# Kernel tuning notes

Hardware: AMD Instinct MI355X
Metric: run time of the kernel (lower is better)

The kernel has to match this reference:

```python
import jax, jax.numpy as jnp
import numpy as np

B, T, S, A = 8, 256, 16, 1
H, NH, L, NI, TIME, TMAX = 1024, 16, 6, 4096, 8, 512
NEG = -10000.0


def _ln(x, g, b, eps=1e-5):
    m = jnp.mean(x, -1, keepdims=True)
    v = jnp.mean((x - m) ** 2, -1, keepdims=True)
    return (x - m) * jax.lax.rsqrt(v + eps) * g + b


def setup_inputs() -> dict:
    key = jax.random.key(0)
    ks = iter(jax.random.split(key, 64))
    w = lambda *s: 0.02 * jax.random.normal(next(ks), s, jnp.float32)
    inp = {
        'states': jax.random.normal(next(ks), (B, T, S), jnp.float32),
        'actions': jax.random.normal(next(ks), (B, T, A), jnp.float32),
        'rtgs': jax.random.normal(next(ks), (B, T, 1), jnp.float32),
        'attention_mask': jnp.ones((B, T, 1), jnp.float32),
        'state_mean': jnp.zeros((S,), jnp.float32),
        'state_std': jnp.ones((S,), jnp.float32),
        'W_es': w(S, H), 'b_es': jnp.zeros((H,)),
        'W_ea': w(A, H), 'b_ea': jnp.zeros((H,)),
        'W_er': w(1, H), 'b_er': jnp.zeros((H,)),
        'E_t': w(TMAX, TIME),
        'W_ts': w(H + TIME, H), 'b_ts': jnp.zeros((H,)),
        'W_ta': w(H + TIME, H), 'b_ta': jnp.zeros((H,)),
        'W_tr': w(H + TIME, H), 'b_tr': jnp.zeros((H,)),
        'eln_g': jnp.ones((H,)), 'eln_b': jnp.zeros((H,)),
        'ln1_g': jnp.ones((L, H)), 'ln1_b': jnp.zeros((L, H)),
        'ln2_g': jnp.ones((L, H)), 'ln2_b': jnp.zeros((L, H)),
        'Wq': w(L, H, H), 'bq': jnp.zeros((L, H)),
        'Wk': w(L, H, H), 'bk': jnp.zeros((L, H)),
        'Wv': w(L, H, H), 'bv': jnp.zeros((L, H)),
        'Wo': w(L, H, H), 'bo': jnp.zeros((L, H)),
        'W1': w(L, H, NI), 'b1': jnp.zeros((L, NI)),
        'W2': w(L, NI, H), 'b2': jnp.zeros((L, H)),
        'W_pa': w(H, A), 'b_pa': jnp.zeros((A,)),
        'timesteps': jax.random.randint(next(ks), (B, T), 0, TMAX),
    }
    return inp


def _forward(states, actions, rtgs, attention_mask, state_mean, state_std,
             W_es, b_es, W_ea, b_ea, W_er, b_er, E_t,
             W_ts, b_ts, W_ta, b_ta, W_tr, b_tr, eln_g, eln_b,
             ln1_g, ln1_b, ln2_g, ln2_b, Wq, bq, Wk, bk, Wv, bv, Wo, bo,
             W1, b1, W2, b2, W_pa, b_pa, timesteps):
    T3 = 3 * T
    dh = H // NH
    s = (states - state_mean) / (state_std + 1e-9)
    te = E_t[timesteps]                                   # [B,T,8]
    se = jnp.concatenate([s @ W_es + b_es, te], -1) @ W_ts + b_ts
    ae = jnp.concatenate([actions @ W_ea + b_ea, te], -1) @ W_ta + b_ta
    re = jnp.concatenate([rtgs @ W_er + b_er, te], -1) @ W_tr + b_tr
    # interleave (rtg, state, action) per timestep -> [B, 3T, H]
    x = jnp.stack([re, se, ae], axis=2).reshape(B, T3, H)
    x = _ln(x, eln_g, eln_b)

    timestep_mask = jnp.max(attention_mask, axis=-1)      # [B,T]
    pad = (1.0 - jnp.repeat(timestep_mask, 3, axis=1)) * NEG  # [B,3T]
    pad = pad[:, None, None, :]
    causal = jnp.tril(jnp.ones((T3, T3), bool))

    def block(x, p):
        (l1g, l1b, wq, bqv, wk, bkv, wv, bvv, wo, bov,
         l2g, l2b, w1, b1v, w2, b2v) = p
        h = _ln(x, l1g, l1b)
        def heads(w, b):
            return (h @ w + b).reshape(B, T3, NH, dh).transpose(0, 2, 1, 3)
        q, k, v = heads(wq, bqv), heads(wk, bkv), heads(wv, bvv)
        att = jnp.einsum('bhqd,bhkd->bhqk', q, k) / jnp.sqrt(jnp.float32(dh))
        att = jnp.where(causal, att, jnp.asarray(NEG, att.dtype)) + pad
        att = jax.nn.softmax(att, axis=-1)
        y = jnp.einsum('bhqk,bhkd->bhqd', att, v)
        y = y.transpose(0, 2, 1, 3).reshape(B, T3, H) @ wo + bov
        x = x + y
        m = _ln(x, l2g, l2b)
        x = x + jax.nn.gelu(m @ w1 + b1v, approximate=False) @ w2 + b2v
        return x, None

    stacked = (ln1_g, ln1_b, Wq, bq, Wk, bk, Wv, bv, Wo, bo,
               ln2_g, ln2_b, W1, b1, W2, b2)
    x, _ = jax.lax.scan(block, x, stacked)

    x = x.reshape(B, T, 3, H)
    action_preds = x[:, :, 1] @ W_pa + b_pa               # state-token positions
    return action_preds


def reference(states, actions, rtgs, attention_mask, state_mean, state_std,
              W_es, b_es, W_ea, b_ea, W_er, b_er, E_t,
              W_ts, b_ts, W_ta, b_ta, W_tr, b_tr, eln_g, eln_b,
              ln1_g, ln1_b, ln2_g, ln2_b, Wq, bq, Wk, bk, Wv, bv, Wo, bo,
              W1, b1, W2, b2, W_pa, b_pa, timesteps):
    return _forward(states, actions, rtgs, attention_mask, state_mean, state_std,
                    W_es, b_es, W_ea, b_ea, W_er, b_er, E_t,
                    W_ts, b_ts, W_ta, b_ta, W_tr, b_tr, eln_g, eln_b,
                    ln1_g, ln1_b, ln2_g, ln2_b, Wq, bq, Wk, bk, Wv, bv, Wo, bo,
                    W1, b1, W2, b2, W_pa, b_pa, timesteps)
```

## Files before the change

### kernel.cpp

```cpp
#include <hip/hip_runtime.h>
#include <math.h>

#define B_    8
#define T_    256
#define S_    16
#define H_    1024
#define NH_   16
#define L_    6
#define NI_   4096
#define TIME_ 8
#define T3_   768
#define DH_   64
#define BT_   2048
#define ROWS_ 6144
#define KE_   1032
#define KEP_  1056
#define NEGV  (-10000.0f)

typedef unsigned short u16;
typedef short bf16x8 __attribute__((ext_vector_type(8)));
typedef float f32x4 __attribute__((ext_vector_type(4)));

__device__ __forceinline__ float bf2f(u16 u) {
    union { unsigned int i; float f; } x; x.i = ((unsigned int)u) << 16; return x.f;
}
__device__ __forceinline__ u16 f2bf(float f) {
    union { float f; unsigned int i; } x; x.f = f;
    unsigned int r = x.i + 0x7FFFu + ((x.i >> 16) & 1u);
    return (u16)(r >> 16);
}
__device__ __forceinline__ float gelu_fast(float x) {
    float y = 0.7978845608028654f * (x + 0.044715f * x * x * x);
    float e = __expf(2.0f * y);
    float t = 1.0f - 2.0f / (e + 1.0f);
    return 0.5f * x * (1.0f + t);
}

__device__ __forceinline__ void gll16(const u16* g, u16* l) {
    __builtin_amdgcn_global_load_lds(
        (const __attribute__((address_space(1))) unsigned int*)g,
        (__attribute__((address_space(3))) unsigned int*)l,
        16, 0, 0);
}

template <int EPI, int BM>
__device__ __forceinline__ void mgemm_core(
    const u16* __restrict__ A, const u16* __restrict__ Bt,
    const float* __restrict__ bias, float* __restrict__ outf,
    u16* __restrict__ outb, const float* __restrict__ res,
    int N, int K, int koff, int klen, bool addb)
{
    constexpr int MT = (BM == 128) ? 4 : 2;
    __shared__ u16 Als[2][BM * 32];
    __shared__ u16 Bls[2][128 * 32];
    const int tid = threadIdx.x;

    const int nbx = N >> 7;
    const int bid = blockIdx.x;
    const int G = nbx << 3;
    const int grp = bid / G;
    const int g = bid - grp * G;
    const int bm = (grp * 8 + (g & 7)) * BM;
    const int bn = (g >> 3) * 128;

    const int lane = tid & 63;
    const int w = tid >> 6;
    const int wr = (BM == 128) ? (w >> 1) : (w & 1);
    const int wc = (BM == 128) ? (w & 1) : (w >> 1);
    const int lrow = lane & 15;
    const int lk = lane >> 4;

    f32x4 acc[MT][4] = {};

    auto stage = [&](int buf, int kk) {
        if (BM == 128) {
            #pragma unroll
            for (int s = 0; s < 2; ++s) {
                const int gb = w * 64 + s * 256;
                const int j = gb >> 7, m0 = gb & 127;
                gll16(A + (size_t)(bm + m0 + lane) * K + kk + j * 8, Als[buf] + gb * 8);
            }
        } else {
            gll16(A + (size_t)(bm + lane) * K + kk + w * 8, Als[buf] + w * 64 * 8);
        }
        #pragma unroll
        for (int s = 0; s < 2; ++s) {
            const int gb = w * 64 + s * 256;
            const int j = gb >> 7, m0 = gb & 127;
            gll16(Bt + (size_t)(bn + m0 + lane) * K + kk + j * 8, Bls[buf] + gb * 8);
        }
    };

    const int niter = klen >> 5;
    stage(0, koff);
    for (int i = 0; i < niter; ++i) {
        __syncthreads();
        if (i + 1 < niter) stage((i + 1) & 1, koff + (i + 1) * 32);
        const bf16x8* Af = (const bf16x8*)Als[i & 1];
        const bf16x8* Bf = (const bf16x8*)Bls[i & 1];
        bf16x8 af[MT], bfr[4];
        #pragma unroll
        for (int tm = 0; tm < MT; ++tm)
            af[tm] = Af[lk * BM + wr * (MT * 16) + tm * 16 + lrow];
        #pragma unroll
        for (int tn = 0; tn < 4; ++tn)
            bfr[tn] = Bf[lk * 128 + wc * 64 + tn * 16 + lrow];
        #pragma unroll
        for (int tm = 0; tm < MT; ++tm)
            #pragma unroll
            for (int tn = 0; tn < 4; ++tn)
                acc[tm][tn] = __builtin_amdgcn_mfma_f32_16x16x32_bf16(
                    af[tm], bfr[tn], acc[tm][tn], 0, 0, 0);
    }

    int cg[4]; float bv[4];
    #pragma unroll
    for (int tn = 0; tn < 4; ++tn) {
        cg[tn] = bn + wc * 64 + tn * 16 + lrow;
        bv[tn] = addb ? bias[cg[tn]] : 0.0f;
    }
    #pragma unroll
    for (int tm = 0; tm < MT; ++tm) {
        const int rbase = bm + wr * (MT * 16) + tm * 16 + lk * 4;
        #pragma unroll
        for (int r = 0; r < 4; ++r) {
            const size_t rowoff = (size_t)(rbase + r) * N;
            #pragma unroll
            for (int tn = 0; tn < 4; ++tn) {
                float v = acc[tm][tn][r] + bv[tn];
                const size_t idx = rowoff + cg[tn];
                if (EPI == 0) outf[idx] = v;
                else if (EPI == 1) outf[idx] = v + res[idx];
                else if (EPI == 2) outb[idx] = f2bf(v);
                else if (EPI == 3) { outb[idx] = f2bf(gelu_fast(v)); }
                else { unsafeAtomicAdd(outf + idx, v); }
            }
        }
    }
}

template <int EPI, int BM>
__global__ __launch_bounds__(256) void mgemm(
    const u16* __restrict__ A, const u16* __restrict__ Bt,
    const float* __restrict__ bias, float* __restrict__ outf,
    u16* __restrict__ outb, const float* __restrict__ res,
    int N, int K)
{
    mgemm_core<EPI, BM>(A, Bt, bias, outf, outb, res, N, K, 0, K, true);
}

template <int EPI, int BM>
__global__ __launch_bounds__(256) void mgemm_sk(
    const u16* __restrict__ A, const u16* __restrict__ Bt,
    const float* __restrict__ bias, float* __restrict__ outf,
    u16* __restrict__ outb, const float* __restrict__ res,
    int N, int K, int nsplit)
{
    const int split = blockIdx.y;
    const int klen = K / nsplit;
    mgemm_core<EPI, BM>(A, Bt, bias, outf, outb, res, N, K,
                        split * klen, klen, split == 0);
}

__global__ __launch_bounds__(256) void mgemm_embed(
    const u16* __restrict__ U, const u16* __restrict__ Wt,
    const float* __restrict__ b0, const float* __restrict__ b1,
    const float* __restrict__ b2, float* __restrict__ out)
{
    const int z = blockIdx.z;
    const float* bias = (z == 0) ? b0 : (z == 1) ? b1 : b2;
    mgemm_core<0, 64>(U + (size_t)z * BT_ * KEP_, Wt + (size_t)z * H_ * KEP_,
                      bias, out + (size_t)z * BT_ * H_, nullptr, nullptr,
                      H_, KEP_, 0, KEP_, true);
}

__device__ __forceinline__ void convT_core(
    const float* __restrict__ W, u16* __restrict__ Wt, int K, int N, int Kpad)
{
    __shared__ float tile[32][65];
    const int k0 = blockIdx.y * 32, n0 = blockIdx.x * 64;
    const int tid = threadIdx.x;
    #pragma unroll
    for (int p = 0; p < 2; ++p) {
        const int kr = (tid >> 4) + p * 16;
        const int nc = (tid & 15) * 4;
        const int k = k0 + kr;
        float4 v = make_float4(0.f, 0.f, 0.f, 0.f);
        if (k < K) v = *(const float4*)(W + (size_t)k * N + n0 + nc);
        tile[kr][nc + 0] = v.x; tile[kr][nc + 1] = v.y;
        tile[kr][nc + 2] = v.z; tile[kr][nc + 3] = v.w;
    }
    __syncthreads();
    #pragma unroll
    for (int p = 0; p < 2; ++p) {
        const int idx = tid + p * 256;
        const int n = idx >> 3, kq = (idx & 7) * 4;
        ushort4 o;
        o.x = f2bf(tile[kq + 0][n]); o.y = f2bf(tile[kq + 1][n]);
        o.z = f2bf(tile[kq + 2][n]); o.w = f2bf(tile[kq + 3][n]);
        *(ushort4*)(Wt + (size_t)(n0 + n) * Kpad + k0 + kq) = o;
    }
}

__global__ __launch_bounds__(256) void convTv(
    const float* __restrict__ W, u16* __restrict__ Wt, int K, int N, int Kpad)
{
    convT_core(W, Wt, K, N, Kpad);
}

__global__ __launch_bounds__(256) void convT_embed(
    const float* __restrict__ W0, const float* __restrict__ W1,
    const float* __restrict__ W2, u16* __restrict__ Wt)
{
    const int z = blockIdx.z;
    const float* W = (z == 0) ? W0 : (z == 1) ? W1 : W2;
    convT_core(W, Wt + (size_t)z * H_ * KEP_, KE_, H_, KEP_);
}

__global__ __launch_bounds__(256) void convT4v(
    const float* __restrict__ Wq, const float* __restrict__ Wk,
    const float* __restrict__ Wv, const float* __restrict__ Wo,
    const float* __restrict__ bq, const float* __restrict__ bk,
    const float* __restrict__ bv,
    u16* __restrict__ WQKVt, u16* __restrict__ Wot, float* __restrict__ bqkv)
{
    const int z = blockIdx.z;
    const float* W = (z == 0) ? Wq : (z == 1) ? Wk : (z == 2) ? Wv : Wo;
    u16* Wt = (z == 3) ? Wot : WQKVt + (size_t)z * H_ * H_;
    convT_core(W, Wt, H_, H_, H_);
    if (blockIdx.x == 0 && blockIdx.y == 0 && z < 3) {
        const float* bsrc = (z == 0) ? bq : (z == 1) ? bk : bv;
        #pragma unroll
        for (int u = 0; u < 4; ++u) {
            int i = threadIdx.x + u * 256;
            bqkv[z * H_ + i] = bsrc[i];
        }
    }
}

__global__ __launch_bounds__(256) void embed_pre_kernel(
    const float* __restrict__ states, const float* __restrict__ actions,
    const float* __restrict__ rtgs, const float* __restrict__ mean,
    const float* __restrict__ stdv, const float* __restrict__ W_es,
    const float* __restrict__ b_es, const float* __restrict__ W_ea,
    const float* __restrict__ b_ea, const float* __restrict__ W_er,
    const float* __restrict__ b_er, const float* __restrict__ E_t,
    const int* __restrict__ timesteps,
    u16* __restrict__ Us, u16* __restrict__ Ua, u16* __restrict__ Ur)
{
    const int bt  = blockIdx.x;
    const int tid = threadIdx.x;
    __shared__ float sn[S_];
    __shared__ float tev[TIME_];
    if (tid < S_) sn[tid] = (states[bt * S_ + tid] - mean[tid]) / (stdv[tid] + 1e-9f);
    if (tid < TIME_) {
        int ts = timesteps[bt];
        tev[tid] = E_t[ts * TIME_ + tid];
    }
    __syncthreads();
    const float av = actions[bt];
    const float rv = rtgs[bt];
    const size_t rowo = (size_t)bt * KEP_;
    #pragma unroll
    for (int u = 0; u < 4; ++u) {
        int n = tid + u * 256;
        float accs = b_es[n];
        #pragma unroll
        for (int i = 0; i < S_; ++i) accs += sn[i] * W_es[i * H_ + n];
        Us[rowo + n] = f2bf(accs);
        Ua[rowo + n] = f2bf(av * W_ea[n] + b_ea[n]);
        Ur[rowo + n] = f2bf(rv * W_er[n] + b_er[n]);
    }
    if (tid < TIME_) {
        u16 tv = f2bf(tev[tid]);
        Us[rowo + H_ + tid] = tv;
        Ua[rowo + H_ + tid] = tv;
        Ur[rowo + H_ + tid] = tv;
    }
    if (tid < KEP_ - KE_) {
        Us[rowo + KE_ + tid] = 0;
        Ua[rowo + KE_ + tid] = 0;
        Ur[rowo + KE_ + tid] = 0;
    }
}

template <bool BF16OUT>
__device__ __forceinline__ void ln_body(const float* __restrict__ src,
                                        const float* __restrict__ g,
                                        const float* __restrict__ b,
                                        void* __restrict__ dst,
                                        float* red, int tid)
{
    float v[4];
    #pragma unroll
    for (int u = 0; u < 4; ++u) v[u] = src[tid + u * 256];
    float s = v[0] + v[1] + v[2] + v[3];
    red[tid] = s; __syncthreads();
    for (int off = 128; off > 0; off >>= 1) {
        if (tid < off) red[tid] += red[tid + off];
        __syncthreads();
    }
    const float mean = red[0] * (1.0f / H_);
    __syncthreads();
    float ss = 0.0f;
    #pragma unroll
    for (int u = 0; u < 4; ++u) { float d = v[u] - mean; ss += d * d; }
    red[tid] = ss; __syncthreads();
    for (int off = 128; off > 0; off >>= 1) {
        if (tid < off) red[tid] += red[tid + off];
        __syncthreads();
    }
    const float var = red[0] * (1.0f / H_);
    const float rs = rsqrtf(var + 1e-5f);
    #pragma unroll
    for (int u = 0; u < 4; ++u) {
        int col = tid + u * 256;
        float y = (v[u] - mean) * rs * g[col] + b[col];
        if (BF16OUT) ((u16*)dst)[col] = f2bf(y);
        else ((float*)dst)[col] = y;
    }
}

__global__ __launch_bounds__(256) void ln_bf16_kernel(
    const float* __restrict__ X, const float* __restrict__ g,
    const float* __restrict__ b, u16* __restrict__ Y)
{
    __shared__ float red[256];
    const size_t row = blockIdx.x;
    ln_body<true>(X + row * H_, g, b, Y + row * H_, red, threadIdx.x);
}

__global__ __launch_bounds__(256) void interleave_eln_kernel(
    const float* __restrict__ RE, const float* __restrict__ SE,
    const float* __restrict__ AE, const float* __restrict__ g,
    const float* __restrict__ b, float* __restrict__ X)
{
    __shared__ float red[256];
    const int row = blockIdx.x;
    const int bi = row / T3_;
    const int rem = row % T3_;
    const int t = rem / 3, slot = rem % 3;
    const float* src = (slot == 0 ? RE : (slot == 1 ? SE : AE)) + (size_t)(bi * T_ + t) * H_;
    ln_body<false>(src, g, b, X + (size_t)row * H_, red, threadIdx.x);
}

__global__ __launch_bounds__(256) void attn_kernel(
    const u16* __restrict__ QKV, const float* __restrict__ amask,
    u16* __restrict__ Y)
{
    const int qt = blockIdx.x;
    const int h  = blockIdx.y;
    const int b  = blockIdx.z;
    const int tid = threadIdx.x;
    const int lane = tid & 63, w = tid >> 6;
    const int l15 = lane & 15, quad = lane >> 4;

    __shared__ u16 Kls[64][72];
    __shared__ u16 Vt[64][72];
    __shared__ u16 Pls[4][16][72];
    __shared__ float padv[64];

    const u16* Qbase = QKV + (size_t)b * T3_ * 3072 + h * 64;
    const u16* Kbase = Qbase + 1024;
    const u16* Vbase = Qbase + 2048;

    bf16x8 qf[2];
    {
        const u16* qp = Qbase + (size_t)(qt * 64 + w * 16 + l15) * 3072 + quad * 8;
        qf[0] = *(const bf16x8*)qp;
        qf[1] = *(const bf16x8*)(qp + 32);
    }

    float m_i[4], l_i[4];
    f32x4 o[4] = {};
    #pragma unroll
    for (int r = 0; r < 4; ++r) { m_i[r] = -3.0e30f; l_i[r] = 0.0f; }

    const int qr0 = qt * 64 + w * 16 + quad * 4;

    for (int kt = 0; kt <= qt; ++kt) {
        #pragma unroll
        for (int s = 0; s < 2; ++s) {
            const int c = tid + s * 256;
            const int tok = c >> 3, cb = c & 7;
            const size_t go = (size_t)(kt * 64 + tok) * 3072 + cb * 8;
            *(uint4*)&Kls[tok][cb * 8] = *(const uint4*)(Kbase + go);
            uint4 vv = *(const uint4*)(Vbase + go);
            const u16* vs = (const u16*)&vv;
            #pragma unroll
            for (int j = 0; j < 8; ++j) Vt[cb * 8 + j][tok] = vs[j];
        }
        if (tid < 64)
            padv[tid] = (1.0f - amask[b * T_ + (kt * 64 + tid) / 3]) * NEGV;
        __syncthreads();

        f32x4 sacc[4];
        #pragma unroll
        for (int nt = 0; nt < 4; ++nt) {
            bf16x8 kf0 = *(const bf16x8*)&Kls[nt * 16 + l15][quad * 8];
            bf16x8 kf1 = *(const bf16x8*)&Kls[nt * 16 + l15][32 + quad * 8];
            f32x4 z = {};
            z = __builtin_amdgcn_mfma_f32_16x16x32_bf16(qf[0], kf0, z, 0, 0, 0);
            sacc[nt] = __builtin_amdgcn_mfma_f32_16x16x32_bf16(qf[1], kf1, z, 0, 0, 0);
        }

        float sv[4][4];
        float rmax[4] = {-3.0e30f, -3.0e30f, -3.0e30f, -3.0e30f};
        #pragma unroll
        for (int nt = 0; nt < 4; ++nt) {
            const int jc = kt * 64 + nt * 16 + l15;
            const float pv = padv[nt * 16 + l15];
            #pragma unroll
            for (int r = 0; r < 4; ++r) {
                float v = (jc <= qr0 + r) ? sacc[nt][r] * 0.125f : NEGV;
                v += pv;
                sv[nt][r] = v;
                rmax[r] = fmaxf(rmax[r], v);
            }
        }
        #pragma unroll
        for (int m = 1; m < 16; m <<= 1)
            #pragma unroll
            for (int r = 0; r < 4; ++r)
                rmax[r] = fmaxf(rmax[r], __shfl_xor(rmax[r], m, 64));
        float al[4], rsum[4];
        #pragma unroll
        for (int r = 0; r < 4; ++r) {
            const float mn = fmaxf(m_i[r], rmax[r]);
            al[r] = __expf(m_i[r] - mn);
            m_i[r] = mn;
            float sum = 0.0f;
            #pragma unroll
            for (int nt = 0; nt < 4; ++nt) {
                float p = __expf(sv[nt][r] - mn);
                sv[nt][r] = p; sum += p;
            }
            rsum[r] = sum;
        }
        #pragma unroll
        for (int m = 1; m < 16; m <<= 1)
            #pragma unroll
            for (int r = 0; r < 4; ++r)
                rsum[r] += __shfl_xor(rsum[r], m, 64);
        #pragma unroll
        for (int r = 0; r < 4; ++r)
            l_i[r] = l_i[r] * al[r] + rsum[r];

        #pragma unroll
        for (int nt = 0; nt < 4; ++nt)
            #pragma unroll
            for (int r = 0; r < 4; ++r)
                Pls[w][quad * 4 + r][nt * 16 + l15] = f2bf(sv[nt][r]);
        #pragma unroll
        for (int dt = 0; dt < 4; ++dt)
            #pragma unroll
            for (int r = 0; r < 4; ++r)
                o[dt][r] *= al[r];

        bf16x8 pf0 = *(const bf16x8*)&Pls[w][l15][quad * 8];
        bf16x8 pf1 = *(const bf16x8*)&Pls[w][l15][32 + quad * 8];
        #pragma unroll
        for (int dt = 0; dt < 4; ++dt) {
            bf16x8 vf0 = *(const bf16x8*)&Vt[dt * 16 + l15][quad * 8];
            bf16x8 vf1 = *(const bf16x8*)&Vt[dt * 16 + l15][32 + quad * 8];
            o[dt] = __builtin_amdgcn_mfma_f32_16x16x32_bf16(pf0, vf0, o[dt], 0, 0, 0);
            o[dt] = __builtin_amdgcn_mfma_f32_16x16x32_bf16(pf1, vf1, o[dt], 0, 0, 0);
        }
        __syncthreads();
    }

    #pragma unroll
    for (int r = 0; r < 4; ++r) {
        const float inv = 1.0f / l_i[r];
        const size_t row = (size_t)b * T3_ + qt * 64 + w * 16 + quad * 4 + r;
        #pragma unroll
        for (int dt = 0; dt < 4; ++dt)
            Y[row * H_ + h * 64 + dt * 16 + l15] = f2bf(o[dt][r] * inv);
    }
}

__global__ __launch_bounds__(256) void head_kernel(
    const float* __restrict__ X, const float* __restrict__ W_pa,
    const float* __restrict__ b_pa, float* __restrict__ out)
{
    __shared__ float red[256];
    const int row = blockIdx.x;
    const int b = row / T_, t = row % T_;
    const float* x = X + ((size_t)b * T3_ + 3 * t + 1) * H_;
    const int tid = threadIdx.x;
    float s = 0.0f;
    #pragma unroll
    for (int u = 0; u < 4; ++u) {
        int col = tid + u * 256;
        s += x[col] * W_pa[col];
    }
    red[tid] = s; __syncthreads();
    for (int off = 128; off > 0; off >>= 1) {
        if (tid < off) red[tid] += red[tid + off];
        __syncthreads();
    }
    if (tid == 0) out[row] = red[0] + b_pa[0];
}

extern "C" void kernel_launch(void* const* d_in, const int* in_sizes, int n_in,
                              void* d_out, int out_size, void* d_ws, size_t ws_size,
                              hipStream_t stream)
{
    const float* states  = (const float*)d_in[0];
    const float* actions = (const float*)d_in[1];
    const float* rtgs    = (const float*)d_in[2];
    const float* amask   = (const float*)d_in[3];
    const float* smean   = (const float*)d_in[4];
    const float* sstd    = (const float*)d_in[5];
    const float* W_es    = (const float*)d_in[6];
    const float* b_es    = (const float*)d_in[7];
    const float* W_ea    = (const float*)d_in[8];
    const float* b_ea    = (const float*)d_in[9];
    const float* W_er    = (const float*)d_in[10];
    const float* b_er    = (const float*)d_in[11];
    const float* E_t     = (const float*)d_in[12];
    const float* W_ts    = (const float*)d_in[13];
    const float* b_ts    = (const float*)d_in[14];
    const float* W_ta    = (const float*)d_in[15];
    const float* b_ta    = (const float*)d_in[16];
    const float* W_tr    = (const float*)d_in[17];
    const float* b_tr    = (const float*)d_in[18];
    const float* eln_g   = (const float*)d_in[19];
    const float* eln_b   = (const float*)d_in[20];
    const float* ln1_g   = (const float*)d_in[21];
    const float* ln1_b   = (const float*)d_in[22];
    const float* ln2_g   = (const float*)d_in[23];
    const float* ln2_b   = (const float*)d_in[24];
    const float* Wq      = (const float*)d_in[25];
    const float* bq      = (const float*)d_in[26];
    const float* Wk      = (const float*)d_in[27];
    const float* bk      = (const float*)d_in[28];
    const float* Wv      = (const float*)d_in[29];
    const float* bv      = (const float*)d_in[30];
    const float* Wo      = (const float*)d_in[31];
    const float* bo      = (const float*)d_in[32];
    const float* W1      = (const float*)d_in[33];
    const float* b1      = (const float*)d_in[34];
    const float* W2      = (const float*)d_in[35];
    const float* b2      = (const float*)d_in[36];
    const float* W_pa    = (const float*)d_in[37];
    const float* b_pa    = (const float*)d_in[38];
    const int*   tsteps  = (const int*)d_in[39];
    float* out = (float*)d_out;

    char* base = (char*)d_ws;
    float* X    = (float*)base;
    u16*   Hb   = (u16*)(base + 25165824);
    u16*   QKVb = (u16*)(base + 37748736);
    u16*   MIDb = (u16*)(base + 75497472);
    u16*   Wbuf = (u16*)(base + 125829120);

    float* bqkv = (float*)MIDb;
    u16* U_s = MIDb;
    u16* U_a = MIDb + (size_t)BT_ * KEP_;
    u16* U_r = MIDb + (size_t)2 * BT_ * KEP_;
    float* SE = (float*)QKVb;
    float* AE = SE + (size_t)BT_ * H_;
    float* RE = AE + (size_t)BT_ * H_;
    u16* Wemb = Wbuf;

    u16* WQKVt = Wbuf;
    u16* Wot   = Wbuf + (size_t)3072 * 1024;
    u16* W1t   = Wbuf + (size_t)4096 * 1024;
    u16* W2t   = Wbuf + (size_t)8192 * 1024;

    embed_pre_kernel<<<BT_, 256, 0, stream>>>(
        states, actions, rtgs, smean, sstd, W_es, b_es, W_ea, b_ea,
        W_er, b_er, E_t, tsteps, U_s, U_a, U_r);

    dim3 gCvE(H_ / 64, KEP_ / 32, 3);
    convT_embed<<<gCvE, 256, 0, stream>>>(W_ts, W_ta, W_tr, Wemb);

    dim3 gEmb((H_ / 128) * (BT_ / 64), 1, 3);
    mgemm_embed<<<gEmb, 256, 0, stream>>>(U_s, Wemb, b_ts, b_ta, b_tr, SE);

    interleave_eln_kernel<<<ROWS_, 256, 0, stream>>>(RE, SE, AE, eln_g, eln_b, X);

    dim3 gCv4(H_ / 64, H_ / 32, 4);
    dim3 gCvM1(NI_ / 64, H_ / 32);
    dim3 gCvM2(H_ / 64, NI_ / 32);
    const int gQKV = (3072 / 128) * (ROWS_ / 128);
    const int gM1  = (NI_ / 128) * (ROWS_ / 128);
    dim3 gOsk((H_ / 128) * (ROWS_ / 128), 2);
    dim3 gAttn(T3_ / 64, NH_, B_);

    for (int l = 0; l < L_; ++l) {
        const size_t wOff = (size_t)l * H_ * H_;
        const size_t bOff = (size_t)l * H_;
        const size_t w1Off = (size_t)l * H_ * NI_;
        const size_t b1Off = (size_t)l * NI_;

        convT4v<<<gCv4, 256, 0, stream>>>(
            Wq + wOff, Wk + wOff, Wv + wOff, Wo + wOff,
            bq + bOff, bk + bOff, bv + bOff, WQKVt, Wot, bqkv);
        convTv<<<gCvM1, 256, 0, stream>>>(W1 + w1Off, W1t, H_, NI_, H_);
        convTv<<<gCvM2, 256, 0, stream>>>(W2 + w1Off, W2t, NI_, H_, NI_);

        ln_bf16_kernel<<<ROWS_, 256, 0, stream>>>(X, ln1_g + bOff, ln1_b + bOff, Hb);
        mgemm<2, 128><<<gQKV, 256, 0, stream>>>(Hb, WQKVt, bqkv, nullptr, QKVb, nullptr, 3072, H_);
        attn_kernel<<<gAttn, 256, 0, stream>>>(QKVb, amask, Hb);
        mgemm_sk<4, 128><<<gOsk, 256, 0, stream>>>(Hb, Wot, bo + bOff, X, nullptr, nullptr, H_, H_, 2);
        ln_bf16_kernel<<<ROWS_, 256, 0, stream>>>(X, ln2_g + bOff, ln2_b + bOff, Hb);
        mgemm<3, 128><<<gM1, 256, 0, stream>>>(Hb, W1t, b1 + b1Off, nullptr, MIDb, nullptr, NI_, H_);
        mgemm_sk<4, 128><<<gOsk, 256, 0, stream>>>(MIDb, W2t, b2 + bOff, X, nullptr, nullptr, H_, NI_, 2);
    }

    head_kernel<<<BT_, 256, 0, stream>>>(X, W_pa, b_pa, out);
}
```

Before: 3.302 ms.

## Merge per-layer weight transposes into one launch and rebalance split-K for O and FFN2

Folds the three per-layer weight-transpose launches (QKV/O, W1, W2) into a single flat-grid kernel that decodes its segment from the block index, which removes launch overhead and tail gaps between kernels. The O projection drops split-K with atomic accumulation and uses a plain GEMM whose epilogue adds the residual in place. The FFN2 GEMM goes from a split-K of 2 to 4 to put more blocks on the device. In exchange there are more atomic adds on X for FFN2 and fewer blocks for the O projection.

```diff
diff --git a/kernel.cpp b/kernel.cpp
--- a/kernel.cpp
+++ b/kernel.cpp
@@ -175,10 +175,11 @@
 }
 
 __device__ __forceinline__ void convT_core(
-    const float* __restrict__ W, u16* __restrict__ Wt, int K, int N, int Kpad)
+    const float* __restrict__ W, u16* __restrict__ Wt,
+    int K, int N, int Kpad, int bx, int by)
 {
     __shared__ float tile[32][65];
-    const int k0 = blockIdx.y * 32, n0 = blockIdx.x * 64;
+    const int k0 = by * 32, n0 = bx * 64;
     const int tid = threadIdx.x;
     #pragma unroll
     for (int p = 0; p < 2; ++p) {
@@ -202,10 +203,38 @@
     }
 }
 
-__global__ __launch_bounds__(256) void convTv(
-    const float* __restrict__ W, u16* __restrict__ Wt, int K, int N, int Kpad)
-{
-    convT_core(W, Wt, K, N, Kpad);
+__global__ __launch_bounds__(256) void convT_layer(
+    const float* __restrict__ Wq, const float* __restrict__ Wk,
+    const float* __restrict__ Wv, const float* __restrict__ Wo,
+    const float* __restrict__ W1, const float* __restrict__ W2,
+    const float* __restrict__ bq, const float* __restrict__ bk,
+    const float* __restrict__ bv,
+    u16* __restrict__ WQKVt, u16* __restrict__ Wot,
+    u16* __restrict__ W1t, u16* __restrict__ W2t, float* __restrict__ bqkv)
+{
+    const int bid = blockIdx.x;
+    const int seg = bid >> 11, r = bid & 2047;
+    if (seg == 0) {
+        const int z = r >> 9, rr = r & 511;
+        const int bx = rr & 15, by = rr >> 4;
+        const float* W = (z == 0) ? Wq : (z == 1) ? Wk : (z == 2) ? Wv : Wo;
+        u16* Wt = (z == 3) ? Wot : WQKVt + (size_t)z * H_ * H_;
+        convT_core(W, Wt, H_, H_, H_, bx, by);
+        if (bx == 0 && by == 0 && z < 3) {
+            const float* bsrc = (z == 0) ? bq : (z == 1) ? bk : bv;
+            #pragma unroll
+            for (int u = 0; u < 4; ++u) {
+                int i = threadIdx.x + u * 256;
+                bqkv[z * H_ + i] = bsrc[i];
+            }
+        }
+    } else if (seg == 1) {
+        const int bx = r & 63, by = r >> 6;
+        convT_core(W1, W1t, H_, NI_, H_, bx, by);
+    } else {
+        const int bx = r & 15, by = r >> 4;
+        convT_core(W2, W2t, NI_, H_, NI_, bx, by);
+    }
 }
 
 __global__ __launch_bounds__(256) void convT_embed(
@@ -214,28 +243,7 @@
 {
     const int z = blockIdx.z;
     const float* W = (z == 0) ? W0 : (z == 1) ? W1 : W2;
-    convT_core(W, Wt + (size_t)z * H_ * KEP_, KE_, H_, KEP_);
-}
-
-__global__ __launch_bounds__(256) void convT4v(
-    const float* __restrict__ Wq, const float* __restrict__ Wk,
-    const float* __restrict__ Wv, const float* __restrict__ Wo,
-    const float* __restrict__ bq, const float* __restrict__ bk,
-    const float* __restrict__ bv,
-    u16* __restrict__ WQKVt, u16* __restrict__ Wot, float* __restrict__ bqkv)
-{
-    const int z = blockIdx.z;
-    const float* W = (z == 0) ? Wq : (z == 1) ? Wk : (z == 2) ? Wv : Wo;
-    u16* Wt = (z == 3) ? Wot : WQKVt + (size_t)z * H_ * H_;
-    convT_core(W, Wt, H_, H_, H_);
-    if (blockIdx.x == 0 && blockIdx.y == 0 && z < 3) {
-        const float* bsrc = (z == 0) ? bq : (z == 1) ? bk : bv;
-        #pragma unroll
-        for (int u = 0; u < 4; ++u) {
-            int i = threadIdx.x + u * 256;
-            bqkv[z * H_ + i] = bsrc[i];
-        }
-    }
+    convT_core(W, Wt + (size_t)z * H_ * KEP_, KE_, H_, KEP_, blockIdx.x, blockIdx.y);
 }
 
 __global__ __launch_bounds__(256) void embed_pre_kernel(
@@ -581,12 +589,10 @@
 
     interleave_eln_kernel<<<ROWS_, 256, 0, stream>>>(RE, SE, AE, eln_g, eln_b, X);
 
-    dim3 gCv4(H_ / 64, H_ / 32, 4);
-    dim3 gCvM1(NI_ / 64, H_ / 32);
-    dim3 gCvM2(H_ / 64, NI_ / 32);
     const int gQKV = (3072 / 128) * (ROWS_ / 128);
+    const int gO   = (H_ / 128) * (ROWS_ / 128);
     const int gM1  = (NI_ / 128) * (ROWS_ / 128);
-    dim3 gOsk((H_ / 128) * (ROWS_ / 128), 2);
+    dim3 gF2sk((H_ / 128) * (ROWS_ / 128), 4);
     dim3 gAttn(T3_ / 64, NH_, B_);
 
     for (int l = 0; l < L_; ++l) {
@@ -595,19 +601,19 @@
         const size_t w1Off = (size_t)l * H_ * NI_;
         const size_t b1Off = (size_t)l * NI_;
 
-        convT4v<<<gCv4, 256, 0, stream>>>(
+        convT_layer<<<6144, 256, 0, stream>>>(
             Wq + wOff, Wk + wOff, Wv + wOff, Wo + wOff,
-            bq + bOff, bk + bOff, bv + bOff, WQKVt, Wot, bqkv);
-        convTv<<<gCvM1, 256, 0, stream>>>(W1 + w1Off, W1t, H_, NI_, H_);
-        convTv<<<gCvM2, 256, 0, stream>>>(W2 + w1Off, W2t, NI_, H_, NI_);
+            W1 + w1Off, W2 + w1Off,
+            bq + bOff, bk + bOff, bv + bOff,
+            WQKVt, Wot, W1t, W2t, bqkv);
 
         ln_bf16_kernel<<<ROWS_, 256, 0, stream>>>(X, ln1_g + bOff, ln1_b + bOff, Hb);
         mgemm<2, 128><<<gQKV, 256, 0, stream>>>(Hb, WQKVt, bqkv, nullptr, QKVb, nullptr, 3072, H_);
         attn_kernel<<<gAttn, 256, 0, stream>>>(QKVb, amask, Hb);
-        mgemm_sk<4, 128><<<gOsk, 256, 0, stream>>>(Hb, Wot, bo + bOff, X, nullptr, nullptr, H_, H_, 2);
+        mgemm<1, 128><<<gO, 256, 0, stream>>>(Hb, Wot, bo + bOff, X, nullptr, X, H_, H_);
         ln_bf16_kernel<<<ROWS_, 256, 0, stream>>>(X, ln2_g + bOff, ln2_b + bOff, Hb);
         mgemm<3, 128><<<gM1, 256, 0, stream>>>(Hb, W1t, b1 + b1Off, nullptr, MIDb, nullptr, NI_, H_);
-        mgemm_sk<4, 128><<<gOsk, 256, 0, stream>>>(MIDb, W2t, b2 + bOff, X, nullptr, nullptr, H_, NI_, 2);
+        mgemm_sk<4, 128><<<gF2sk, 256, 0, stream>>>(MIDb, W2t, b2 + bOff, X, nullptr, nullptr, H_, NI_, 4);
     }
 
     head_kernel<<<BT_, 256, 0, stream>>>(X, W_pa, b_pa, out);
```

Measured after the change: 3.274 ms. About the same (-0.9%).
